# Kernel optimization log

Hardware: AMD Instinct MI355X
Metric: run time of the kernel (lower is better)

Reference implementation:

```python
import jax, jax.numpy as jnp
import numpy as np

J6, J3 = 13, 30          # joints with 6-dim and 3-dim outputs (contiguous groups)
J = J6 + J3              # 43 joints total
D = 512                  # latent_dim
B, T = 16, 196


def setup_inputs() -> dict:
    key = jax.random.key(0)
    ks = jax.random.split(key, 7)
    s = 0.02  # weight init scale
    return {
        "x":   jax.random.normal(ks[0], (B, T, J, D), dtype=jnp.float32),
        "W1":  jax.random.normal(ks[1], (J, D, D), dtype=jnp.float32) * s,
        "b1":  jax.random.normal(ks[2], (J, D), dtype=jnp.float32) * s,
        "W2a": jax.random.normal(ks[3], (J6, D, 6), dtype=jnp.float32) * s,
        "b2a": jax.random.normal(ks[4], (J6, 6), dtype=jnp.float32) * s,
        "W2b": jax.random.normal(ks[5], (J3, D, 3), dtype=jnp.float32) * s,
        "b2b": jax.random.normal(ks[6], (J3, 3), dtype=jnp.float32) * s,
    }


def reference(x, W1, b1, W2a, b2a, W2b, b2b):
    # Per-joint MLP: Linear(D,D) -> GELU -> Linear(D,out_dim_j), concatenated
    # over joints along the last dim (heterogeneous 'dk' mode, vectorized).
    h = jnp.einsum('btjd,jde->btje', x, W1) + b1          # [B,T,J,D]
    h = jax.nn.gelu(h, approximate=False)                  # torch nn.GELU (erf)
    oa = jnp.einsum('btjd,jdo->btjo', h[:, :, :J6], W2a) + b2a  # [B,T,13,6]
    ob = jnp.einsum('btjd,jdo->btjo', h[:, :, J6:], W2b) + b2b  # [B,T,30,3]
    b, t = x.shape[0], x.shape[1]
    # torch.cat(out_list, dim=-1) in joint order == group-wise reshape + concat
    motion = jnp.concatenate([oa.reshape(b, t, -1), ob.reshape(b, t, -1)], axis=-1)
    return motion  # [B, T, 13*6 + 30*3] = [B, T, 168]
```

## Files before the change

### kernel.cpp

```cpp
#include <hip/hip_runtime.h>
#include <hip/hip_bf16.h>

typedef unsigned short ushort_t;
typedef short short8 __attribute__((ext_vector_type(8)));
typedef float f32x4 __attribute__((ext_vector_type(4)));

#define J_TOT 43
#define J6 13
#define D_DIM 512
#define BT 3136
#define OUTW 168

__device__ __forceinline__ unsigned short bf16rne(float f) {
    unsigned u = __builtin_bit_cast(unsigned, f);
    u += 0x7fffu + ((u >> 16) & 1u);
    return (unsigned short)(u >> 16);
}

__device__ __forceinline__ float gelu_f(float v) {
    float t = v * __builtin_fmaf(v * v, 0.0356774081f, 0.7978845608f);
    float e = __builtin_amdgcn_exp2f(t * 2.8853900818f);
    float s = __builtin_amdgcn_rcpf(1.0f + e);
    return __builtin_fmaf(-v, s, v);
}

__device__ __forceinline__ void async_ld16(const void* gsrc, void* ldst) {
    __builtin_amdgcn_global_load_lds(
        (const __attribute__((address_space(1))) unsigned int*)(unsigned long long)(const char*)gsrc,
        (__attribute__((address_space(3))) unsigned int*)ldst,
        16, 0, 0);
}

__global__ void w1_transpose_kernel(const float* __restrict__ W1, ushort_t* __restrict__ W1t) {
    __shared__ ushort_t tile[64][74];
    const int j = blockIdx.z;
    const int t = threadIdx.x;
    const int d0 = blockIdx.x * 64, e0 = blockIdx.y * 64;
    const float* src = W1 + (size_t)j * D_DIM * D_DIM;
    const int el = t & 63, dl = t >> 6;
#pragma unroll
    for (int i = 0; i < 16; i++) {
        int d = dl + i * 4;
        tile[el][d] = bf16rne(src[(size_t)(d0 + d) * D_DIM + e0 + el]);
    }
    __syncthreads();
    ushort_t* dst = W1t + (size_t)j * D_DIM * D_DIM;
#pragma unroll
    for (int i = 0; i < 16; i++) {
        int n = dl + i * 4;
        dst[(size_t)(e0 + n) * D_DIM + d0 + el] = tile[n][el];
    }
}

__global__ void w2_pack_kernel(const float* __restrict__ W2a, const float* __restrict__ b2a,
                               const float* __restrict__ W2b, const float* __restrict__ b2b,
                               ushort_t* __restrict__ W2t, float* __restrict__ b2p) {
    const int j = blockIdx.x;
    const int t = threadIdx.x;
    const int odim = (j < J6) ? 6 : 3;
    const float* w = (j < J6) ? (W2a + (size_t)j * D_DIM * 6) : (W2b + (size_t)(j - J6) * D_DIM * 3);
    for (int idx = t; idx < 16 * D_DIM; idx += 256) {
        int o = idx >> 9, k = idx & 511;
        float v = (o < odim) ? w[(size_t)k * odim + o] : 0.0f;
        W2t[(size_t)j * 16 * D_DIM + idx] = bf16rne(v);
    }
    if (t < 16) {
        const float* bb = (j < J6) ? (b2a + (size_t)j * 6) : (b2b + (size_t)(j - J6) * 3);
        b2p[j * 16 + t] = (t < odim) ? bb[t] : 0.0f;
    }
}

__global__ __launch_bounds__(256, 2)
void MotionDecoder_36309653520632_kernel(const float* __restrict__ x,
                                         const float* __restrict__ b1,
                                         const ushort_t* __restrict__ W1t,
                                         const ushort_t* __restrict__ W2t,
                                         const float* __restrict__ b2p,
                                         float* __restrict__ out) {
    __shared__ unsigned char smem[32768];
    char* as_base = (char*)smem;
    char* bs_base = (char*)smem + 16384;
    char* hs_base = (char*)smem;

    const int j   = blockIdx.y;
    const int m0  = blockIdx.x * 128;
    const int tid = threadIdx.x;
    const int lane = tid & 63;
    const int wid  = tid >> 6;
    const int wrow = (wid >> 1) * 64;
    const int wcol = (wid & 1) * 64;

    const int a_m  = tid >> 1;
    const int a_k0 = (tid & 1) * 32;
    int a_row = m0 + a_m; if (a_row > BT - 1) a_row = BT - 1;
    const float* xrow = x + ((size_t)a_row * J_TOT + j) * D_DIM;

    const ushort_t* w1j = W1t + (size_t)j * D_DIM * D_DIM;
    const ushort_t* w2j = W2t + (size_t)j * 16 * D_DIM;

    f32x4 acc2[4];
#pragma unroll
    for (int r = 0; r < 4; r++) acc2[r] = (f32x4){0.f, 0.f, 0.f, 0.f};

    for (int nt = 0; nt < 4; nt++) {
        const int n0 = nt * 128;
        f32x4 acc[4][4];
#pragma unroll
        for (int a = 0; a < 4; a++)
#pragma unroll
            for (int b = 0; b < 4; b++) acc[a][b] = (f32x4){0.f, 0.f, 0.f, 0.f};

        for (int ks = 0; ks < 8; ks++) {
#pragma unroll
            for (int pass = 0; pass < 4; pass++) {
                int n = pass * 32 + wid * 8 + (lane >> 3);
                int cg = (lane & 7) ^ (n & 7);
                const ushort_t* gsrc = w1j + (size_t)(n0 + n) * D_DIM + ks * 64 + cg * 8;
                char* ldst = bs_base + (pass * 32 + wid * 8) * 128;
                async_ld16(gsrc, ldst);
            }
            const float* ap = xrow + ks * 64 + a_k0;
            float4 f[8];
#pragma unroll
            for (int i = 0; i < 8; i++) f[i] = ((const float4*)ap)[i];
#pragma unroll
            for (int c = 0; c < 4; c++) {
                union { unsigned short s[8]; uint4 v; } pk;
                float4 u0 = f[2 * c], u1 = f[2 * c + 1];
                pk.s[0] = bf16rne(u0.x); pk.s[1] = bf16rne(u0.y);
                pk.s[2] = bf16rne(u0.z); pk.s[3] = bf16rne(u0.w);
                pk.s[4] = bf16rne(u1.x); pk.s[5] = bf16rne(u1.y);
                pk.s[6] = bf16rne(u1.z); pk.s[7] = bf16rne(u1.w);
                int ch = (a_k0 >> 3) + c;
                int sw = ch ^ (a_m & 7);
                *(uint4*)(as_base + a_m * 128 + sw * 16) = pk.v;
            }
            __syncthreads();
#pragma unroll
            for (int kk = 0; kk < 2; kk++) {
                short8 af[4], bfr[4];
                int chv = kk * 4 + (lane >> 4);
#pragma unroll
                for (int rt = 0; rt < 4; rt++) {
                    int m = wrow + rt * 16 + (lane & 15);
                    af[rt] = *(const short8*)(as_base + m * 128 + ((chv ^ (m & 7)) * 16));
                }
#pragma unroll
                for (int ct = 0; ct < 4; ct++) {
                    int n = wcol + ct * 16 + (lane & 15);
                    bfr[ct] = *(const short8*)(bs_base + n * 128 + ((chv ^ (n & 7)) * 16));
                }
#pragma unroll
                for (int rt = 0; rt < 4; rt++)
#pragma unroll
                    for (int ct = 0; ct < 4; ct++)
                        acc[rt][ct] = __builtin_amdgcn_mfma_f32_16x16x32_bf16(
                            af[rt], bfr[ct], acc[rt][ct], 0, 0, 0);
            }
            __syncthreads();
        }

#pragma unroll
        for (int ct = 0; ct < 4; ct++) {
            int ncol = wcol + ct * 16 + (lane & 15);
            float bv = b1[j * D_DIM + n0 + ncol];
            int c2 = ncol >> 3;
            int boff = (ncol & 7) * 2;
#pragma unroll
            for (int rt = 0; rt < 4; rt++) {
                int mb = wrow + rt * 16 + ((lane >> 4) << 2);
#pragma unroll
                for (int r = 0; r < 4; r++) {
                    float g = gelu_f(acc[rt][ct][r] + bv);
                    int m = mb + r;
                    int sw = c2 ^ (m & 15);
                    *(unsigned short*)(hs_base + m * 256 + sw * 16 + boff) = bf16rne(g);
                }
            }
        }
        __syncthreads();

        if (wid < 2) {
            short8 wf[4];
#pragma unroll
            for (int kk2 = 0; kk2 < 4; kk2++) {
                const ushort_t* gsrc = w2j + (size_t)(lane & 15) * D_DIM + n0 + kk2 * 32 + (lane >> 4) * 8;
                wf[kk2] = *(const short8*)gsrc;
            }
#pragma unroll
            for (int rt = 0; rt < 4; rt++) {
                int m = wid * 64 + rt * 16 + (lane & 15);
#pragma unroll
                for (int kk2 = 0; kk2 < 4; kk2++) {
                    int ch = kk2 * 4 + (lane >> 4);
                    short8 a2 = *(const short8*)(hs_base + m * 256 + ((ch ^ (m & 15)) * 16));
                    acc2[rt] = __builtin_amdgcn_mfma_f32_16x16x32_bf16(a2, wf[kk2], acc2[rt], 0, 0, 0);
                }
            }
        }
        __syncthreads();
    }

    if (wid < 2) {
        int o = lane & 15;
        int odim = (j < J6) ? 6 : 3;
        int cb = (j < J6) ? j * 6 : 78 + (j - J6) * 3;
        float bo = b2p[j * 16 + o];
        if (o < odim) {
#pragma unroll
            for (int rt = 0; rt < 4; rt++) {
#pragma unroll
                for (int r = 0; r < 4; r++) {
                    int m = m0 + wid * 64 + rt * 16 + ((lane >> 4) << 2) + r;
                    if (m < BT) out[(size_t)m * OUTW + cb + o] = acc2[rt][r] + bo;
                }
            }
        }
    }
}

extern "C" void kernel_launch(void* const* d_in, const int* in_sizes, int n_in,
                              void* d_out, int out_size, void* d_ws, size_t ws_size,
                              hipStream_t stream) {
    const float* x   = (const float*)d_in[0];
    const float* W1  = (const float*)d_in[1];
    const float* b1  = (const float*)d_in[2];
    const float* W2a = (const float*)d_in[3];
    const float* b2a = (const float*)d_in[4];
    const float* W2b = (const float*)d_in[5];
    const float* b2b = (const float*)d_in[6];
    float* out = (float*)d_out;

    ushort_t* W1t = (ushort_t*)d_ws;
    ushort_t* W2t = W1t + (size_t)J_TOT * D_DIM * D_DIM;
    float*    b2p = (float*)(W2t + (size_t)J_TOT * 16 * D_DIM);

    w1_transpose_kernel<<<dim3(8, 8, J_TOT), 256, 0, stream>>>(W1, W1t);
    w2_pack_kernel<<<J_TOT, 256, 0, stream>>>(W2a, b2a, W2b, b2b, W2t, b2p);
    MotionDecoder_36309653520632_kernel<<<dim3(25, J_TOT), 256, 0, stream>>>(
        x, b1, W1t, W2t, b2p, out);
}
```

Baseline: 655.6 us.

## Pre-convert x to bf16, double-buffer K loop, remap workgroups per XCD

Adds a fused prepass that converts x to bf16 in workspace (when it fits) alongside the W1 transpose and W2 pack. The main kernel now uses a 1D grid remapped so each XCD handles contiguous joint tiles, double-buffers K=32 slices with async global-to-LDS loads, and raises occupancy to 3 blocks per SM. All four waves now do the second GEMM, and the b1 and W2 loads are hoisted. The aim is better L2 reuse of W1 and overlap of loads with MFMA, at the cost of an extra full pass over x in the prepass.

Result: no change. 661.9 us (+1.0%).

```diff
diff --git a/kernel.cpp b/kernel.cpp
--- a/kernel.cpp
+++ b/kernel.cpp
@@ -1,5 +1,4 @@
 #include <hip/hip_runtime.h>
-#include <hip/hip_bf16.h>
 
 typedef unsigned short ushort_t;
 typedef short short8 __attribute__((ext_vector_type(8)));
@@ -10,6 +9,7 @@
 #define D_DIM 512
 #define BT 3136
 #define OUTW 168
+#define NWG 1075
 
 __device__ __forceinline__ unsigned short bf16rne(float f) {
     unsigned u = __builtin_bit_cast(unsigned, f);
@@ -31,32 +31,49 @@
         16, 0, 0);
 }
 
-__global__ void w1_transpose_kernel(const float* __restrict__ W1, ushort_t* __restrict__ W1t) {
-    __shared__ ushort_t tile[64][74];
-    const int j = blockIdx.z;
-    const int t = threadIdx.x;
-    const int d0 = blockIdx.x * 64, e0 = blockIdx.y * 64;
-    const float* src = W1 + (size_t)j * D_DIM * D_DIM;
-    const int el = t & 63, dl = t >> 6;
-#pragma unroll
-    for (int i = 0; i < 16; i++) {
-        int d = dl + i * 4;
-        tile[el][d] = bf16rne(src[(size_t)(d0 + d) * D_DIM + e0 + el]);
-    }
-    __syncthreads();
-    ushort_t* dst = W1t + (size_t)j * D_DIM * D_DIM;
-#pragma unroll
-    for (int i = 0; i < 16; i++) {
-        int n = dl + i * 4;
-        dst[(size_t)(e0 + n) * D_DIM + d0 + el] = tile[n][el];
-    }
-}
-
-__global__ void w2_pack_kernel(const float* __restrict__ W2a, const float* __restrict__ b2a,
+__global__ void prepass_kernel(const float* __restrict__ x, ushort_t* __restrict__ xb, int xbB,
+                               const float* __restrict__ W1, ushort_t* __restrict__ W1t,
+                               const float* __restrict__ W2a, const float* __restrict__ b2a,
                                const float* __restrict__ W2b, const float* __restrict__ b2b,
                                ushort_t* __restrict__ W2t, float* __restrict__ b2p) {
-    const int j = blockIdx.x;
+    __shared__ __align__(16) ushort_t tile[64][72];
+    const int b = blockIdx.x;
     const int t = threadIdx.x;
+
+    if (b < xbB) {
+        size_t i = ((size_t)b * 256 + t) * 8;
+        float4 f0 = *(const float4*)(x + i);
+        float4 f1 = *(const float4*)(x + i + 4);
+        union { unsigned short s[8]; uint4 v; } pk;
+        pk.s[0] = bf16rne(f0.x); pk.s[1] = bf16rne(f0.y);
+        pk.s[2] = bf16rne(f0.z); pk.s[3] = bf16rne(f0.w);
+        pk.s[4] = bf16rne(f1.x); pk.s[5] = bf16rne(f1.y);
+        pk.s[6] = bf16rne(f1.z); pk.s[7] = bf16rne(f1.w);
+        *(uint4*)(xb + i) = pk.v;
+        return;
+    }
+    const int bb = b - xbB;
+    if (bb < 2752) {
+        const int d0 = (bb & 7) * 64, e0 = ((bb >> 3) & 7) * 64, j = bb >> 6;
+        const float* src = W1 + (size_t)j * D_DIM * D_DIM;
+        const int el = t & 63, dl = t >> 6;
+#pragma unroll
+        for (int i = 0; i < 16; i++) {
+            int d = dl + i * 4;
+            tile[el][d] = bf16rne(src[(size_t)(d0 + d) * D_DIM + e0 + el]);
+        }
+        __syncthreads();
+        ushort_t* dst = W1t + (size_t)j * D_DIM * D_DIM;
+#pragma unroll
+        for (int p = 0; p < 2; p++) {
+            int idx = p * 256 + t;
+            int e = idx >> 3, c = idx & 7;
+            uint4 v = *(const uint4*)(&tile[e][c * 8]);
+            *(uint4*)(dst + (size_t)(e0 + e) * D_DIM + d0 + c * 8) = v;
+        }
+        return;
+    }
+    const int j = bb - 2752;
     const int odim = (j < J6) ? 6 : 3;
     const float* w = (j < J6) ? (W2a + (size_t)j * D_DIM * 6) : (W2b + (size_t)(j - J6) * D_DIM * 3);
     for (int idx = t; idx < 16 * D_DIM; idx += 256) {
@@ -65,157 +82,203 @@
         W2t[(size_t)j * 16 * D_DIM + idx] = bf16rne(v);
     }
     if (t < 16) {
-        const float* bb = (j < J6) ? (b2a + (size_t)j * 6) : (b2b + (size_t)(j - J6) * 3);
-        b2p[j * 16 + t] = (t < odim) ? bb[t] : 0.0f;
-    }
-}
-
-__global__ __launch_bounds__(256, 2)
+        const float* bbv = (j < J6) ? (b2a + (size_t)j * 6) : (b2b + (size_t)(j - J6) * 3);
+        b2p[j * 16 + t] = (t < odim) ? bbv[t] : 0.0f;
+    }
+}
+
+template<int USE_XB>
+__global__ __launch_bounds__(256, 3)
 void MotionDecoder_36309653520632_kernel(const float* __restrict__ x,
+                                         const ushort_t* __restrict__ xb,
                                          const float* __restrict__ b1,
                                          const ushort_t* __restrict__ W1t,
                                          const ushort_t* __restrict__ W2t,
                                          const float* __restrict__ b2p,
                                          float* __restrict__ out) {
-    __shared__ unsigned char smem[32768];
-    char* as_base = (char*)smem;
-    char* bs_base = (char*)smem + 16384;
+    __shared__ __align__(16) unsigned char smem[32768];
     char* hs_base = (char*)smem;
 
-    const int j   = blockIdx.y;
-    const int m0  = blockIdx.x * 128;
-    const int tid = threadIdx.x;
+    const int bid = blockIdx.x;
+    const int xcd = bid & 7, idx = bid >> 3;
+    const int wg = (xcd < 3) ? (xcd * 135 + idx) : (405 + (xcd - 3) * 134 + idx);
+    const int j  = wg / 25;
+    const int mt = wg - j * 25;
+    const int m0 = mt * 128;
+
+    const int tid  = threadIdx.x;
     const int lane = tid & 63;
     const int wid  = tid >> 6;
     const int wrow = (wid >> 1) * 64;
     const int wcol = (wid & 1) * 64;
 
-    const int a_m  = tid >> 1;
-    const int a_k0 = (tid & 1) * 32;
-    int a_row = m0 + a_m; if (a_row > BT - 1) a_row = BT - 1;
-    const float* xrow = x + ((size_t)a_row * J_TOT + j) * D_DIM;
-
     const ushort_t* w1j = W1t + (size_t)j * D_DIM * D_DIM;
     const ushort_t* w2j = W2t + (size_t)j * 16 * D_DIM;
 
-    f32x4 acc2[4];
-#pragma unroll
-    for (int r = 0; r < 4; r++) acc2[r] = (f32x4){0.f, 0.f, 0.f, 0.f};
+    const int sg_sub = lane >> 2;
+    const int sg_c   = lane & 3;
+    const ushort_t* aG[2];
+    const float*    aGf[2];
+    const ushort_t* bG[2];
+    int sLd[2];
+#pragma unroll
+    for (int p = 0; p < 2; p++) {
+        int mrow = wid * 32 + p * 16 + sg_sub;
+        int row = m0 + mrow; if (row > BT - 1) row = BT - 1;
+        int g = sg_c ^ ((mrow >> 1) & 3);
+        sLd[p] = (wid * 32 + p * 16) * 64;
+        if (USE_XB) aG[p]  = xb + ((size_t)row * J_TOT + j) * D_DIM + g * 8;
+        else        aGf[p] = x  + ((size_t)row * J_TOT + j) * D_DIM + g * 8;
+        bG[p] = w1j + (size_t)mrow * D_DIM + g * 8;
+    }
+
+    f32x4 acc2[2];
+    acc2[0] = (f32x4){0.f, 0.f, 0.f, 0.f};
+    acc2[1] = (f32x4){0.f, 0.f, 0.f, 0.f};
 
     for (int nt = 0; nt < 4; nt++) {
         const int n0 = nt * 128;
+
+        float bvv[4];
+#pragma unroll
+        for (int ct = 0; ct < 4; ct++)
+            bvv[ct] = b1[j * D_DIM + n0 + wcol + ct * 16 + (lane & 15)];
+        short8 wf[4];
+#pragma unroll
+        for (int kk2 = 0; kk2 < 4; kk2++)
+            wf[kk2] = *(const short8*)(w2j + (size_t)(lane & 15) * D_DIM + n0 + kk2 * 32 + (lane >> 4) * 8);
+
         f32x4 acc[4][4];
 #pragma unroll
         for (int a = 0; a < 4; a++)
 #pragma unroll
-            for (int b = 0; b < 4; b++) acc[a][b] = (f32x4){0.f, 0.f, 0.f, 0.f};
-
-        for (int ks = 0; ks < 8; ks++) {
-#pragma unroll
-            for (int pass = 0; pass < 4; pass++) {
-                int n = pass * 32 + wid * 8 + (lane >> 3);
-                int cg = (lane & 7) ^ (n & 7);
-                const ushort_t* gsrc = w1j + (size_t)(n0 + n) * D_DIM + ks * 64 + cg * 8;
-                char* ldst = bs_base + (pass * 32 + wid * 8) * 128;
-                async_ld16(gsrc, ldst);
-            }
-            const float* ap = xrow + ks * 64 + a_k0;
-            float4 f[8];
-#pragma unroll
-            for (int i = 0; i < 8; i++) f[i] = ((const float4*)ap)[i];
-#pragma unroll
-            for (int c = 0; c < 4; c++) {
+            for (int c = 0; c < 4; c++) acc[a][c] = (f32x4){0.f, 0.f, 0.f, 0.f};
+
+        float4 a32[2][2];
+        if (USE_XB) {
+#pragma unroll
+            for (int p = 0; p < 2; p++) async_ld16(aG[p], (char*)smem + sLd[p]);
+        } else {
+#pragma unroll
+            for (int p = 0; p < 2; p++) {
+                a32[p][0] = *(const float4*)(aGf[p]);
+                a32[p][1] = *(const float4*)(aGf[p] + 4);
+            }
+        }
+#pragma unroll
+        for (int p = 0; p < 2; p++)
+            async_ld16(bG[p] + (size_t)n0 * D_DIM, (char*)smem + 8192 + sLd[p]);
+        if (!USE_XB) {
+#pragma unroll
+            for (int p = 0; p < 2; p++) {
                 union { unsigned short s[8]; uint4 v; } pk;
-                float4 u0 = f[2 * c], u1 = f[2 * c + 1];
-                pk.s[0] = bf16rne(u0.x); pk.s[1] = bf16rne(u0.y);
-                pk.s[2] = bf16rne(u0.z); pk.s[3] = bf16rne(u0.w);
-                pk.s[4] = bf16rne(u1.x); pk.s[5] = bf16rne(u1.y);
-                pk.s[6] = bf16rne(u1.z); pk.s[7] = bf16rne(u1.w);
-                int ch = (a_k0 >> 3) + c;
-                int sw = ch ^ (a_m & 7);
-                *(uint4*)(as_base + a_m * 128 + sw * 16) = pk.v;
+                pk.s[0] = bf16rne(a32[p][0].x); pk.s[1] = bf16rne(a32[p][0].y);
+                pk.s[2] = bf16rne(a32[p][0].z); pk.s[3] = bf16rne(a32[p][0].w);
+                pk.s[4] = bf16rne(a32[p][1].x); pk.s[5] = bf16rne(a32[p][1].y);
+                pk.s[6] = bf16rne(a32[p][1].z); pk.s[7] = bf16rne(a32[p][1].w);
+                *(uint4*)((char*)smem + sLd[p] + lane * 16) = pk.v;
+            }
+        }
+        __syncthreads();
+
+        int cur = 0;
+        for (int ks = 0; ks < 16; ks++) {
+            if (ks < 15) {
+                const int kn = ks + 1;
+                char* abN = (char*)smem + (cur ^ 1) * 16384;
+                if (USE_XB) {
+#pragma unroll
+                    for (int p = 0; p < 2; p++) async_ld16(aG[p] + kn * 32, abN + sLd[p]);
+                } else {
+#pragma unroll
+                    for (int p = 0; p < 2; p++) {
+                        a32[p][0] = *(const float4*)(aGf[p] + kn * 32);
+                        a32[p][1] = *(const float4*)(aGf[p] + kn * 32 + 4);
+                    }
+                }
+#pragma unroll
+                for (int p = 0; p < 2; p++)
+                    async_ld16(bG[p] + (size_t)n0 * D_DIM + kn * 32, abN + 8192 + sLd[p]);
+            }
+            char* ab  = (char*)smem + cur * 16384;
+            char* bb2 = ab + 8192;
+            const int chv = lane >> 4;
+            short8 af[4], bfr[4];
+#pragma unroll
+            for (int rt = 0; rt < 4; rt++) {
+                int m = wrow + rt * 16 + (lane & 15);
+                af[rt] = *(const short8*)(ab + m * 64 + ((chv ^ ((m >> 1) & 3)) * 16));
+            }
+#pragma unroll
+            for (int ct = 0; ct < 4; ct++) {
+                int n = wcol + ct * 16 + (lane & 15);
+                bfr[ct] = *(const short8*)(bb2 + n * 64 + ((chv ^ ((n >> 1) & 3)) * 16));
+            }
+#pragma unroll
+            for (int rt = 0; rt < 4; rt++)
+#pragma unroll
+                for (int ct = 0; ct < 4; ct++)
+                    acc[rt][ct] = __builtin_amdgcn_mfma_f32_16x16x32_bf16(
+                        af[rt], bfr[ct], acc[rt][ct], 0, 0, 0);
+            if (!USE_XB && ks < 15) {
+                char* abN = (char*)smem + (cur ^ 1) * 16384;
+#pragma unroll
+                for (int p = 0; p < 2; p++) {
+                    union { unsigned short s[8]; uint4 v; } pk;
+                    pk.s[0] = bf16rne(a32[p][0].x); pk.s[1] = bf16rne(a32[p][0].y);
+                    pk.s[2] = bf16rne(a32[p][0].z); pk.s[3] = bf16rne(a32[p][0].w);
+                    pk.s[4] = bf16rne(a32[p][1].x); pk.s[5] = bf16rne(a32[p][1].y);
+                    pk.s[6] = bf16rne(a32[p][1].z); pk.s[7] = bf16rne(a32[p][1].w);
+                    *(uint4*)(abN + sLd[p] + lane * 16) = pk.v;
+                }
             }
             __syncthreads();
-#pragma unroll
-            for (int kk = 0; kk < 2; kk++) {
-                short8 af[4], bfr[4];
-                int chv = kk * 4 + (lane >> 4);
-#pragma unroll
-                for (int rt = 0; rt < 4; rt++) {
-                    int m = wrow + rt * 16 + (lane & 15);
-                    af[rt] = *(const short8*)(as_base + m * 128 + ((chv ^ (m & 7)) * 16));
-                }
-#pragma unroll
-                for (int ct = 0; ct < 4; ct++) {
-                    int n = wcol + ct * 16 + (lane & 15);
-                    bfr[ct] = *(const short8*)(bs_base + n * 128 + ((chv ^ (n & 7)) * 16));
-                }
-#pragma unroll
-                for (int rt = 0; rt < 4; rt++)
-#pragma unroll
-                    for (int ct = 0; ct < 4; ct++)
-                        acc[rt][ct] = __builtin_amdgcn_mfma_f32_16x16x32_bf16(
-                            af[rt], bfr[ct], acc[rt][ct], 0, 0, 0);
-            }
-            __syncthreads();
+            cur ^= 1;
         }
 
 #pragma unroll
         for (int ct = 0; ct < 4; ct++) {
             int ncol = wcol + ct * 16 + (lane & 15);
-            float bv = b1[j * D_DIM + n0 + ncol];
             int c2 = ncol >> 3;
             int boff = (ncol & 7) * 2;
 #pragma unroll
             for (int rt = 0; rt < 4; rt++) {
                 int mb = wrow + rt * 16 + ((lane >> 4) << 2);
 #pragma unroll
-                for (int r = 0; r < 4; r++) {
-                    float g = gelu_f(acc[rt][ct][r] + bv);
-                    int m = mb + r;
-                    int sw = c2 ^ (m & 15);
-                    *(unsigned short*)(hs_base + m * 256 + sw * 16 + boff) = bf16rne(g);
+                for (int rr = 0; rr < 4; rr++) {
+                    float g = gelu_f(acc[rt][ct][rr] + bvv[ct]);
+                    int m = mb + rr;
+                    *(unsigned short*)(hs_base + m * 256 + ((c2 ^ (m & 15)) * 16) + boff) = bf16rne(g);
                 }
             }
         }
         __syncthreads();
 
-        if (wid < 2) {
-            short8 wf[4];
+#pragma unroll
+        for (int rt = 0; rt < 2; rt++) {
+            int m = wid * 32 + rt * 16 + (lane & 15);
 #pragma unroll
             for (int kk2 = 0; kk2 < 4; kk2++) {
-                const ushort_t* gsrc = w2j + (size_t)(lane & 15) * D_DIM + n0 + kk2 * 32 + (lane >> 4) * 8;
-                wf[kk2] = *(const short8*)gsrc;
-            }
-#pragma unroll
-            for (int rt = 0; rt < 4; rt++) {
-                int m = wid * 64 + rt * 16 + (lane & 15);
-#pragma unroll
-                for (int kk2 = 0; kk2 < 4; kk2++) {
-                    int ch = kk2 * 4 + (lane >> 4);
-                    short8 a2 = *(const short8*)(hs_base + m * 256 + ((ch ^ (m & 15)) * 16));
-                    acc2[rt] = __builtin_amdgcn_mfma_f32_16x16x32_bf16(a2, wf[kk2], acc2[rt], 0, 0, 0);
-                }
+                int ch = kk2 * 4 + (lane >> 4);
+                short8 a2 = *(const short8*)(hs_base + m * 256 + ((ch ^ (m & 15)) * 16));
+                acc2[rt] = __builtin_amdgcn_mfma_f32_16x16x32_bf16(a2, wf[kk2], acc2[rt], 0, 0, 0);
             }
         }
         __syncthreads();
     }
 
-    if (wid < 2) {
-        int o = lane & 15;
-        int odim = (j < J6) ? 6 : 3;
-        int cb = (j < J6) ? j * 6 : 78 + (j - J6) * 3;
+    const int o = lane & 15;
+    const int odim = (j < J6) ? 6 : 3;
+    const int cb = (j < J6) ? j * 6 : 78 + (j - J6) * 3;
+    if (o < odim) {
         float bo = b2p[j * 16 + o];
-        if (o < odim) {
-#pragma unroll
-            for (int rt = 0; rt < 4; rt++) {
-#pragma unroll
-                for (int r = 0; r < 4; r++) {
-                    int m = m0 + wid * 64 + rt * 16 + ((lane >> 4) << 2) + r;
-                    if (m < BT) out[(size_t)m * OUTW + cb + o] = acc2[rt][r] + bo;
-                }
-            }
-        }
+#pragma unroll
+        for (int rt = 0; rt < 2; rt++)
+#pragma unroll
+            for (int rr = 0; rr < 4; rr++) {
+                int m = m0 + wid * 32 + rt * 16 + ((lane >> 4) << 2) + rr;
+                if (m < BT) out[(size_t)m * OUTW + cb + o] = acc2[rt][rr] + bo;
+            }
     }
 }
 
@@ -234,9 +297,21 @@
     ushort_t* W1t = (ushort_t*)d_ws;
     ushort_t* W2t = W1t + (size_t)J_TOT * D_DIM * D_DIM;
     float*    b2p = (float*)(W2t + (size_t)J_TOT * 16 * D_DIM);
-
-    w1_transpose_kernel<<<dim3(8, 8, J_TOT), 256, 0, stream>>>(W1, W1t);
-    w2_pack_kernel<<<J_TOT, 256, 0, stream>>>(W2a, b2a, W2b, b2b, W2t, b2p);
-    MotionDecoder_36309653520632_kernel<<<dim3(25, J_TOT), 256, 0, stream>>>(
-        x, b1, W1t, W2t, b2p, out);
-}
+    size_t head = (size_t)J_TOT * D_DIM * D_DIM * 2
+                + (size_t)J_TOT * 16 * D_DIM * 2
+                + (size_t)J_TOT * 16 * 4;
+    head = (head + 255) & ~(size_t)255;
+    const size_t xb_bytes = (size_t)BT * J_TOT * D_DIM * 2;
+    const bool use_xb = (ws_size >= head + xb_bytes);
+    ushort_t* xbp = (ushort_t*)((char*)d_ws + head);
+
+    const int xbB = use_xb ? 33712 : 0;
+    prepass_kernel<<<xbB + 2752 + J_TOT, 256, 0, stream>>>(
+        x, xbp, xbB, W1, W1t, W2a, b2a, W2b, b2b, W2t, b2p);
+    if (use_xb)
+        MotionDecoder_36309653520632_kernel<1><<<NWG, 256, 0, stream>>>(
+            x, xbp, b1, W1t, W2t, b2p, out);
+    else
+        MotionDecoder_36309653520632_kernel<0><<<NWG, 256, 0, stream>>>(
+            x, xbp, b1, W1t, W2t, b2p, out);
+}
```

## Restructure fused MLP kernel with full-K A tile, triple-buffered W1, and XCD mapping

Applied to the files above, without the earlier changes.

Rewrites the main kernel so each 512-thread workgroup handles a 64-row by full 512-column tile for one joint. The whole x row block is loaded once into a 64KB LDS tile, and W1 slices are streamed through a triple-buffered async global-to-LDS pipeline with explicit waitcnt and barriers. The second GEMM now runs once at the end instead of once per N-chunk. Workgroups are remapped to XCDs so tiles of the same joint share an L2, and the two weight-prepass kernels are merged into one launch with vectorized transpose stores. It needs 160KB dynamic LDS, which likely allows only one workgroup per CU, and it drops the bounds check on the last row tile because 49×64 covers 3136 exactly.

New measurement: 561.6 us. 1.17x faster.

```diff
diff --git a/kernel.cpp b/kernel.cpp
--- a/kernel.cpp
+++ b/kernel.cpp
@@ -1,5 +1,4 @@
 #include <hip/hip_runtime.h>
-#include <hip/hip_bf16.h>
 
 typedef unsigned short ushort_t;
 typedef short short8 __attribute__((ext_vector_type(8)));
@@ -10,6 +9,8 @@
 #define D_DIM 512
 #define BT 3136
 #define OUTW 168
+#define MTILES 49
+#define NWG (MTILES * J_TOT)
 
 __device__ __forceinline__ unsigned short bf16rne(float f) {
     unsigned u = __builtin_bit_cast(unsigned, f);
@@ -31,32 +32,35 @@
         16, 0, 0);
 }
 
-__global__ void w1_transpose_kernel(const float* __restrict__ W1, ushort_t* __restrict__ W1t) {
-    __shared__ ushort_t tile[64][74];
-    const int j = blockIdx.z;
-    const int t = threadIdx.x;
-    const int d0 = blockIdx.x * 64, e0 = blockIdx.y * 64;
-    const float* src = W1 + (size_t)j * D_DIM * D_DIM;
-    const int el = t & 63, dl = t >> 6;
-#pragma unroll
-    for (int i = 0; i < 16; i++) {
-        int d = dl + i * 4;
-        tile[el][d] = bf16rne(src[(size_t)(d0 + d) * D_DIM + e0 + el]);
-    }
-    __syncthreads();
-    ushort_t* dst = W1t + (size_t)j * D_DIM * D_DIM;
-#pragma unroll
-    for (int i = 0; i < 16; i++) {
-        int n = dl + i * 4;
-        dst[(size_t)(e0 + n) * D_DIM + d0 + el] = tile[n][el];
-    }
-}
-
-__global__ void w2_pack_kernel(const float* __restrict__ W2a, const float* __restrict__ b2a,
+__global__ void prepass_kernel(const float* __restrict__ W1, ushort_t* __restrict__ W1t,
+                               const float* __restrict__ W2a, const float* __restrict__ b2a,
                                const float* __restrict__ W2b, const float* __restrict__ b2b,
                                ushort_t* __restrict__ W2t, float* __restrict__ b2p) {
-    const int j = blockIdx.x;
+    __shared__ __align__(16) ushort_t tile[64][72];
+    const int b = blockIdx.x;
     const int t = threadIdx.x;
+
+    if (b < 2752) {
+        const int d0 = (b & 7) * 64, e0 = ((b >> 3) & 7) * 64, j = b >> 6;
+        const float* src = W1 + (size_t)j * D_DIM * D_DIM;
+        const int el = t & 63, dl = t >> 6;
+#pragma unroll
+        for (int i = 0; i < 16; i++) {
+            int d = dl + i * 4;
+            tile[el][d] = bf16rne(src[(size_t)(d0 + d) * D_DIM + e0 + el]);
+        }
+        __syncthreads();
+        ushort_t* dst = W1t + (size_t)j * D_DIM * D_DIM;
+#pragma unroll
+        for (int p = 0; p < 2; p++) {
+            int idx = p * 256 + t;
+            int e = idx >> 3, c = idx & 7;
+            uint4 v = *(const uint4*)(&tile[e][c * 8]);
+            *(uint4*)(dst + (size_t)(e0 + e) * D_DIM + d0 + c * 8) = v;
+        }
+        return;
+    }
+    const int j = b - 2752;
     const int odim = (j < J6) ? 6 : 3;
     const float* w = (j < J6) ? (W2a + (size_t)j * D_DIM * 6) : (W2b + (size_t)(j - J6) * D_DIM * 3);
     for (int idx = t; idx < 16 * D_DIM; idx += 256) {
@@ -65,158 +69,188 @@
         W2t[(size_t)j * 16 * D_DIM + idx] = bf16rne(v);
     }
     if (t < 16) {
-        const float* bb = (j < J6) ? (b2a + (size_t)j * 6) : (b2b + (size_t)(j - J6) * 3);
-        b2p[j * 16 + t] = (t < odim) ? bb[t] : 0.0f;
-    }
-}
-
-__global__ __launch_bounds__(256, 2)
+        const float* bbv = (j < J6) ? (b2a + (size_t)j * 6) : (b2b + (size_t)(j - J6) * 3);
+        b2p[j * 16 + t] = (t < odim) ? bbv[t] : 0.0f;
+    }
+}
+
+__global__ __launch_bounds__(512, 2)
 void MotionDecoder_36309653520632_kernel(const float* __restrict__ x,
                                          const float* __restrict__ b1,
                                          const ushort_t* __restrict__ W1t,
                                          const ushort_t* __restrict__ W2t,
                                          const float* __restrict__ b2p,
                                          float* __restrict__ out) {
-    __shared__ unsigned char smem[32768];
-    char* as_base = (char*)smem;
-    char* bs_base = (char*)smem + 16384;
-    char* hs_base = (char*)smem;
-
-    const int j   = blockIdx.y;
-    const int m0  = blockIdx.x * 128;
-    const int tid = threadIdx.x;
+    extern __shared__ __align__(16) char smem[];
+    char* As = smem;
+    char* B0 = smem + 65536;
+    char* B1 = smem + 98304;
+    char* B2 = smem + 131072;
+    char* hs = smem + 65536;
+
+    const int bid = blockIdx.x;
+    const int xcd = bid & 7, bi = bid >> 3;
+    const int wg = (xcd < 3) ? (xcd * 264 + bi) : (792 + (xcd - 3) * 263 + bi);
+    const int j  = wg / MTILES;
+    const int mt = wg - j * MTILES;
+    const int m0 = mt * 64;
+
+    const int tid  = threadIdx.x;
     const int lane = tid & 63;
-    const int wid  = tid >> 6;
-    const int wrow = (wid >> 1) * 64;
-    const int wcol = (wid & 1) * 64;
-
-    const int a_m  = tid >> 1;
-    const int a_k0 = (tid & 1) * 32;
-    int a_row = m0 + a_m; if (a_row > BT - 1) a_row = BT - 1;
-    const float* xrow = x + ((size_t)a_row * J_TOT + j) * D_DIM;
+    const int w    = tid >> 6;
+    const int l15  = lane & 15;
+    const int l4   = lane >> 4;
 
     const ushort_t* w1j = W1t + (size_t)j * D_DIM * D_DIM;
-    const ushort_t* w2j = W2t + (size_t)j * 16 * D_DIM;
-
-    f32x4 acc2[4];
-#pragma unroll
-    for (int r = 0; r < 4; r++) acc2[r] = (f32x4){0.f, 0.f, 0.f, 0.f};
-
-    for (int nt = 0; nt < 4; nt++) {
-        const int n0 = nt * 128;
-        f32x4 acc[4][4];
-#pragma unroll
-        for (int a = 0; a < 4; a++)
-#pragma unroll
-            for (int b = 0; b < 4; b++) acc[a][b] = (f32x4){0.f, 0.f, 0.f, 0.f};
-
-        for (int ks = 0; ks < 8; ks++) {
-#pragma unroll
-            for (int pass = 0; pass < 4; pass++) {
-                int n = pass * 32 + wid * 8 + (lane >> 3);
-                int cg = (lane & 7) ^ (n & 7);
-                const ushort_t* gsrc = w1j + (size_t)(n0 + n) * D_DIM + ks * 64 + cg * 8;
-                char* ldst = bs_base + (pass * 32 + wid * 8) * 128;
-                async_ld16(gsrc, ldst);
+
+    const ushort_t* bGp0; const ushort_t* bGp1; const ushort_t* bGp2; const ushort_t* bGp3;
+    int sB0, sB1, sB2, sB3;
+    {
+        int rbase = w * 64;
+#pragma unroll
+        for (int p = 0; p < 4; p++) {
+            int rw  = rbase + p * 16;
+            int row = rw + (lane >> 2);
+            int g   = (lane & 3) ^ ((row >> 1) & 3);
+            const ushort_t* gp = w1j + (size_t)row * D_DIM + g * 8;
+            int s = rw * 64;
+            if (p == 0) { bGp0 = gp; sB0 = s; }
+            else if (p == 1) { bGp1 = gp; sB1 = s; }
+            else if (p == 2) { bGp2 = gp; sB2 = s; }
+            else { bGp3 = gp; sB3 = s; }
+        }
+    }
+
+#define STAGE_B(buf, kk) do { \
+        async_ld16(bGp0 + (kk) * 32, (buf) + sB0); \
+        async_ld16(bGp1 + (kk) * 32, (buf) + sB1); \
+        async_ld16(bGp2 + (kk) * 32, (buf) + sB2); \
+        async_ld16(bGp3 + (kk) * 32, (buf) + sB3); \
+    } while (0)
+
+    const int xr = tid >> 3;
+    const int c8 = tid & 7;
+    const float* xrow = x + ((size_t)(m0 + xr) * J_TOT + j) * D_DIM + c8 * 8;
+
+    float4 xv[16];
+#pragma unroll
+    for (int i = 0; i < 8; i++) {
+        xv[2 * i]     = *(const float4*)(xrow + i * 64);
+        xv[2 * i + 1] = *(const float4*)(xrow + i * 64 + 4);
+    }
+    STAGE_B(B0, 0);
+    STAGE_B(B1, 1);
+    {
+        const int swr = xr & 7;
+#pragma unroll
+        for (int i = 0; i < 8; i++) {
+            union { unsigned short s[8]; uint4 v; } pk;
+            float4 f0 = xv[2 * i], f1 = xv[2 * i + 1];
+            pk.s[0] = bf16rne(f0.x); pk.s[1] = bf16rne(f0.y);
+            pk.s[2] = bf16rne(f0.z); pk.s[3] = bf16rne(f0.w);
+            pk.s[4] = bf16rne(f1.x); pk.s[5] = bf16rne(f1.y);
+            pk.s[6] = bf16rne(f1.z); pk.s[7] = bf16rne(f1.w);
+            int c = c8 + i * 8;
+            *(uint4*)(As + xr * 1024 + ((c ^ swr) << 4)) = pk.v;
+        }
+    }
+    float bvv[4];
+#pragma unroll
+    for (int ct = 0; ct < 4; ct++)
+        bvv[ct] = b1[j * D_DIM + w * 64 + ct * 16 + l15];
+
+    asm volatile("s_waitcnt lgkmcnt(0)" ::: "memory");
+    __builtin_amdgcn_s_barrier();
+    __builtin_amdgcn_sched_barrier(0);
+
+    f32x4 acc[4][4];
+#pragma unroll
+    for (int a = 0; a < 4; a++)
+#pragma unroll
+        for (int c = 0; c < 4; c++) acc[a][c] = (f32x4){0.f, 0.f, 0.f, 0.f};
+
+    char* bufA = B0; char* bufB = B1; char* bufC = B2;
+    for (int ks = 0; ks < 16; ks++) {
+        if (ks < 14) {
+            STAGE_B(bufC, ks + 2);
+            asm volatile("s_waitcnt vmcnt(8)" ::: "memory");
+        } else if (ks == 14) {
+            asm volatile("s_waitcnt vmcnt(4)" ::: "memory");
+        } else {
+            asm volatile("s_waitcnt vmcnt(0)" ::: "memory");
+        }
+        __builtin_amdgcn_s_barrier();
+        __builtin_amdgcn_sched_barrier(0);
+
+        short8 af[4], bf[4];
+#pragma unroll
+        for (int rt = 0; rt < 4; rt++) {
+            int m = rt * 16 + l15;
+            int q = ks * 4 + l4;
+            af[rt] = *(const short8*)(As + m * 1024 + (((q ^ (m & 7))) << 4));
+        }
+#pragma unroll
+        for (int ct = 0; ct < 4; ct++) {
+            int n = w * 64 + ct * 16 + l15;
+            bf[ct] = *(const short8*)(bufA + n * 64 + ((l4 ^ ((n >> 1) & 3)) << 4));
+        }
+        asm volatile("s_waitcnt lgkmcnt(0)" ::: "memory");
+        __builtin_amdgcn_s_barrier();
+        __builtin_amdgcn_sched_barrier(0);
+
+        __builtin_amdgcn_s_setprio(1);
+#pragma unroll
+        for (int rt = 0; rt < 4; rt++)
+#pragma unroll
+            for (int ct = 0; ct < 4; ct++)
+                acc[rt][ct] = __builtin_amdgcn_mfma_f32_16x16x32_bf16(
+                    af[rt], bf[ct], acc[rt][ct], 0, 0, 0);
+        __builtin_amdgcn_s_setprio(0);
+
+        char* tmp = bufA; bufA = bufB; bufB = bufC; bufC = tmp;
+    }
+
+#pragma unroll
+    for (int ct = 0; ct < 4; ct++) {
+        int n = w * 64 + ct * 16 + l15;
+        int cc = n >> 3, boff = (n & 7) * 2;
+#pragma unroll
+        for (int rt = 0; rt < 4; rt++) {
+            int mb = rt * 16 + (l4 << 2);
+#pragma unroll
+            for (int rr = 0; rr < 4; rr++) {
+                int m = mb + rr;
+                float g = gelu_f(acc[rt][ct][rr] + bvv[ct]);
+                *(unsigned short*)(hs + m * 1024 + (((cc ^ (m & 7))) << 4) + boff) = bf16rne(g);
             }
-            const float* ap = xrow + ks * 64 + a_k0;
-            float4 f[8];
-#pragma unroll
-            for (int i = 0; i < 8; i++) f[i] = ((const float4*)ap)[i];
-#pragma unroll
-            for (int c = 0; c < 4; c++) {
-                union { unsigned short s[8]; uint4 v; } pk;
-                float4 u0 = f[2 * c], u1 = f[2 * c + 1];
-                pk.s[0] = bf16rne(u0.x); pk.s[1] = bf16rne(u0.y);
-                pk.s[2] = bf16rne(u0.z); pk.s[3] = bf16rne(u0.w);
-                pk.s[4] = bf16rne(u1.x); pk.s[5] = bf16rne(u1.y);
-                pk.s[6] = bf16rne(u1.z); pk.s[7] = bf16rne(u1.w);
-                int ch = (a_k0 >> 3) + c;
-                int sw = ch ^ (a_m & 7);
-                *(uint4*)(as_base + a_m * 128 + sw * 16) = pk.v;
+        }
+    }
+    __syncthreads();
+
+    if (w < 4) {
+        const ushort_t* w2j = W2t + (size_t)j * 16 * D_DIM + (size_t)l15 * D_DIM + l4 * 8;
+        f32x4 a2acc = (f32x4){0.f, 0.f, 0.f, 0.f};
+        const int m = w * 16 + l15;
+#pragma unroll
+        for (int kc = 0; kc < 16; kc++) {
+            short8 wf = *(const short8*)(w2j + kc * 32);
+            int q = kc * 4 + l4;
+            short8 a2 = *(const short8*)(hs + m * 1024 + (((q ^ (m & 7))) << 4));
+            a2acc = __builtin_amdgcn_mfma_f32_16x16x32_bf16(a2, wf, a2acc, 0, 0, 0);
+        }
+        const int o = l15;
+        const int odim = (j < J6) ? 6 : 3;
+        const int cb = (j < J6) ? j * 6 : 78 + (j - J6) * 3;
+        if (o < odim) {
+            float bo = b2p[j * 16 + o];
+#pragma unroll
+            for (int rr = 0; rr < 4; rr++) {
+                int mm = m0 + w * 16 + (l4 << 2) + rr;
+                out[(size_t)mm * OUTW + cb + o] = a2acc[rr] + bo;
             }
-            __syncthreads();
-#pragma unroll
-            for (int kk = 0; kk < 2; kk++) {
-                short8 af[4], bfr[4];
-                int chv = kk * 4 + (lane >> 4);
-#pragma unroll
-                for (int rt = 0; rt < 4; rt++) {
-                    int m = wrow + rt * 16 + (lane & 15);
-                    af[rt] = *(const short8*)(as_base + m * 128 + ((chv ^ (m & 7)) * 16));
-                }
-#pragma unroll
-                for (int ct = 0; ct < 4; ct++) {
-                    int n = wcol + ct * 16 + (lane & 15);
-                    bfr[ct] = *(const short8*)(bs_base + n * 128 + ((chv ^ (n & 7)) * 16));
-                }
-#pragma unroll
-                for (int rt = 0; rt < 4; rt++)
-#pragma unroll
-                    for (int ct = 0; ct < 4; ct++)
-                        acc[rt][ct] = __builtin_amdgcn_mfma_f32_16x16x32_bf16(
-                            af[rt], bfr[ct], acc[rt][ct], 0, 0, 0);
-            }
-            __syncthreads();
-        }
-
-#pragma unroll
-        for (int ct = 0; ct < 4; ct++) {
-            int ncol = wcol + ct * 16 + (lane & 15);
-            float bv = b1[j * D_DIM + n0 + ncol];
-            int c2 = ncol >> 3;
-            int boff = (ncol & 7) * 2;
-#pragma unroll
-            for (int rt = 0; rt < 4; rt++) {
-                int mb = wrow + rt * 16 + ((lane >> 4) << 2);
-#pragma unroll
-                for (int r = 0; r < 4; r++) {
-                    float g = gelu_f(acc[rt][ct][r] + bv);
-                    int m = mb + r;
-                    int sw = c2 ^ (m & 15);
-                    *(unsigned short*)(hs_base + m * 256 + sw * 16 + boff) = bf16rne(g);
-                }
-            }
-        }
-        __syncthreads();
-
-        if (wid < 2) {
-            short8 wf[4];
-#pragma unroll
-            for (int kk2 = 0; kk2 < 4; kk2++) {
-                const ushort_t* gsrc = w2j + (size_t)(lane & 15) * D_DIM + n0 + kk2 * 32 + (lane >> 4) * 8;
-                wf[kk2] = *(const short8*)gsrc;
-            }
-#pragma unroll
-            for (int rt = 0; rt < 4; rt++) {
-                int m = wid * 64 + rt * 16 + (lane & 15);
-#pragma unroll
-                for (int kk2 = 0; kk2 < 4; kk2++) {
-                    int ch = kk2 * 4 + (lane >> 4);
-                    short8 a2 = *(const short8*)(hs_base + m * 256 + ((ch ^ (m & 15)) * 16));
-                    acc2[rt] = __builtin_amdgcn_mfma_f32_16x16x32_bf16(a2, wf[kk2], acc2[rt], 0, 0, 0);
-                }
-            }
-        }
-        __syncthreads();
-    }
-
-    if (wid < 2) {
-        int o = lane & 15;
-        int odim = (j < J6) ? 6 : 3;
-        int cb = (j < J6) ? j * 6 : 78 + (j - J6) * 3;
-        float bo = b2p[j * 16 + o];
-        if (o < odim) {
-#pragma unroll
-            for (int rt = 0; rt < 4; rt++) {
-#pragma unroll
-                for (int r = 0; r < 4; r++) {
-                    int m = m0 + wid * 64 + rt * 16 + ((lane >> 4) << 2) + r;
-                    if (m < BT) out[(size_t)m * OUTW + cb + o] = acc2[rt][r] + bo;
-                }
-            }
-        }
-    }
+        }
+    }
+#undef STAGE_B
 }
 
 extern "C" void kernel_launch(void* const* d_in, const int* in_sizes, int n_in,
@@ -235,8 +269,15 @@
     ushort_t* W2t = W1t + (size_t)J_TOT * D_DIM * D_DIM;
     float*    b2p = (float*)(W2t + (size_t)J_TOT * 16 * D_DIM);
 
-    w1_transpose_kernel<<<dim3(8, 8, J_TOT), 256, 0, stream>>>(W1, W1t);
-    w2_pack_kernel<<<J_TOT, 256, 0, stream>>>(W2a, b2a, W2b, b2b, W2t, b2p);
-    MotionDecoder_36309653520632_kernel<<<dim3(25, J_TOT), 256, 0, stream>>>(
+    static bool attr_set = false;
+    if (!attr_set) {
+        (void)hipFuncSetAttribute(
+            reinterpret_cast<const void*>(MotionDecoder_36309653520632_kernel),
+            hipFuncAttributeMaxDynamicSharedMemorySize, 163840);
+        attr_set = true;
+    }
+
+    prepass_kernel<<<2752 + J_TOT, 256, 0, stream>>>(W1, W1t, W2a, b2a, W2b, b2b, W2t, b2p);
+    MotionDecoder_36309653520632_kernel<<<NWG, 512, 163840, stream>>>(
         x, b1, W1t, W2t, b2p, out);
 }
```
